# Optimization experiments

Measured on AMD Instinct MI355X. Metric: run time of the kernel, lower is better.

## Reference

```python
import jax, jax.numpy as jnp
import numpy as np

B, S, E, H, V, C = 256, 20, 512, 512, 32000, 1000


def _lstm_step(x, h, c, W, U, b):
    # Keras LSTM, activation='relu', recurrent_activation='sigmoid', gate order i,f,c,o
    z = x @ W + h @ U + b  # (B, 4H)
    i, f, g, o = jnp.split(z, 4, axis=-1)
    i = jax.nn.sigmoid(i)
    f = jax.nn.sigmoid(f)
    g = jax.nn.relu(g)
    o = jax.nn.sigmoid(o)
    c_new = f * c + i * g
    h_new = o * jax.nn.relu(c_new)
    return h_new, c_new


def setup_inputs() -> dict:
    key = jax.random.key(0)
    ks = jax.random.split(key, 24)
    std = 0.05
    d_in1 = S * E + 2 * E  # flattened encoder output + word embed + speaker embed
    inp = {
        "encoded_output": jax.random.normal(ks[0], (B, S, E), jnp.float32),
        "word_embedding": jax.random.normal(ks[1], (B, E), jnp.float32),
        "h0": jax.random.normal(ks[2], (B, H), jnp.float32) * std,
        "c0": jax.random.normal(ks[3], (B, H), jnp.float32) * std,
        "speaker": jax.random.randint(ks[4], (B,), 0, C),
        "addressee": jax.random.randint(ks[5], (B,), 0, C),
        "persona_emb": jax.random.normal(ks[6], (C, E), jnp.float32) * 0.1,
        "W1": jax.random.normal(ks[7], (d_in1, 4 * H), jnp.float32) * std,
        "U1": jax.random.normal(ks[8], (H, 4 * H), jnp.float32) * std,
        "b1": jnp.zeros((4 * H,), jnp.float32),
        "W2": jax.random.normal(ks[9], (H, 4 * H), jnp.float32) * std,
        "U2": jax.random.normal(ks[10], (H, 4 * H), jnp.float32) * std,
        "b2": jnp.zeros((4 * H,), jnp.float32),
        "W3": jax.random.normal(ks[11], (H, 4 * H), jnp.float32) * std,
        "U3": jax.random.normal(ks[12], (H, 4 * H), jnp.float32) * std,
        "b3": jnp.zeros((4 * H,), jnp.float32),
        "W4": jax.random.normal(ks[13], (H, 4 * H), jnp.float32) * std,
        "U4": jax.random.normal(ks[14], (H, 4 * H), jnp.float32) * std,
        "b4": jnp.zeros((4 * H,), jnp.float32),
        "Wd": jax.random.normal(ks[15], (H, V), jnp.float32) * std,
        "bd": jnp.zeros((V,), jnp.float32),
    }
    return inp


def reference(encoded_output, word_embedding, h0, c0, speaker, addressee,
              persona_emb, W1, U1, b1, W2, U2, b2, W3, U3, b3, W4, U4, b4, Wd, bd):
    b = encoded_output.shape[0]
    # The Python double loop in the original is exactly: (B,S,E) -> (B, S*E)
    enc_flat = encoded_output.reshape(b, -1)
    speaker_embed = persona_emb[speaker]  # (B, E)
    # is_speaker=True branch: concat [flattened encoder, word embed, speaker embed]
    x = jnp.concatenate([enc_flat, word_embedding, speaker_embed], axis=-1)
    # seq length is 1, so each LSTM layer is a single cell step;
    # each layer's initial state is the previous layer's final (h, c)
    h1, c1 = _lstm_step(x, h0, c0, W1, U1, b1)
    h2, c2 = _lstm_step(h1, h1, c1, W2, U2, b2)
    h3, c3 = _lstm_step(h2, h2, c2, W3, U3, b3)
    h4, c4 = _lstm_step(h3, h3, c3, W4, U4, b4)
    probs = jax.nn.softmax(h4 @ Wd + bd, axis=-1)  # (B, V)
    return probs, (h4, c4)
```

## Files before the change

### kernel.cpp

```cpp
#include <hip/hip_runtime.h>
#include <cstdint>
#include <cmath>

typedef _Float16 f16;
typedef _Float16 f16x8 __attribute__((ext_vector_type(8)));
typedef _Float16 f16x4 __attribute__((ext_vector_type(4)));
typedef float f32x4 __attribute__((ext_vector_type(4)));

__device__ inline void gld_lds16(const void* g, void* l) {
  __builtin_amdgcn_global_load_lds(
      (__attribute__((address_space(1))) void*)(uintptr_t)g,
      (__attribute__((address_space(3))) void*)l, 16, 0, 0);
}

__global__ __launch_bounds__(256) void build_x1_kernel(
    const float* __restrict__ enc, const float* __restrict__ word,
    const float* __restrict__ pers, const int* __restrict__ speaker,
    const float* __restrict__ h0, f16* __restrict__ X)
{
  const int b  = blockIdx.y;
  const int k2 = blockIdx.x * 256 + threadIdx.x;
  const int k  = k2 * 2;
  float v0, v1;
  if (k < 10240) {
    const float* p = enc + (long long)b * 10240 + k; v0 = p[0]; v1 = p[1];
  } else if (k < 10752) {
    const float* p = word + b * 512 + (k - 10240);   v0 = p[0]; v1 = p[1];
  } else if (k < 11264) {
    const float* p = pers + (long long)speaker[b] * 512 + (k - 10752); v0 = p[0]; v1 = p[1];
  } else {
    const float* p = h0 + b * 512 + (k - 11264);     v0 = p[0]; v1 = p[1];
  }
  union { f16 h[2]; unsigned int u; } pk;
  pk.h[0] = (f16)v0; pk.h[1] = (f16)v1;
  ((unsigned int*)X)[(long long)b * 5888 + k2] = pk.u;
}

__global__ __launch_bounds__(256) void wsum_t_kernel(
    const float* __restrict__ W2, const float* __restrict__ U2,
    const float* __restrict__ W3, const float* __restrict__ U3,
    const float* __restrict__ W4, const float* __restrict__ U4,
    f16* __restrict__ out)
{
  const int t = blockIdx.x * 256 + threadIdx.x;
  const int L = blockIdx.y;
  const float* W = (L == 0) ? W2 : (L == 1) ? W3 : W4;
  const float* U = (L == 0) ? U2 : (L == 1) ? U3 : U4;
  const int n  = t & 2047;
  const int k0 = (t >> 11) << 6;
  f16* op = out + (long long)L * (2048 * 512) + (long long)n * 512 + k0;
  for (int kk = 0; kk < 64; kk += 8) {
    f16x8 v;
    #pragma unroll
    for (int j = 0; j < 8; j++) {
      const int k = k0 + kk + j;
      v[j] = (f16)(W[(long long)k * 2048 + n] + U[(long long)k * 2048 + n]);
    }
    *(f16x8*)(op + kk) = v;
  }
}

__global__ __launch_bounds__(256, 2) void gemm_pipe2(
    const f16* __restrict__ A, int lda,
    const float* __restrict__ B0, const float* __restrict__ B1, int ksw, int ldb,
    void* __restrict__ Cv, int ldc, long long c_split_stride, int niter,
    int store_f16)
{
  __shared__ __align__(16) f16 Ah[2][256 * 32];
  __shared__ __align__(16) f16 Bh[2][128 * 40];

  const int tid  = threadIdx.x;
  const int lane = tid & 63;
  const int wave = tid >> 6;
  const int n0 = blockIdx.x * 128;
  const int kbeg = blockIdx.y * (niter * 32);

  const int a_row16 = lane >> 2;
  const int a_ksub  = ((lane & 3) ^ ((lane >> 3) & 3)) * 8;

  const int nl0  = (tid & 63) * 2;
  const int koct = tid >> 6;

  float2 bv[8];

  auto issueB = [&](int kt) {
    const int kb = kbeg + kt * 32 + koct * 8;
    #pragma unroll
    for (int i = 0; i < 8; i++) {
      const int krow = kb + i;
      const float* bp = (krow >= ksw) ? (B1 + (long long)(krow - ksw) * ldb)
                                      : (B0 + (long long)krow * ldb);
      bv[i] = *(const float2*)(bp + n0 + nl0);
    }
  };
  auto issueA = [&](int kt) {
    const int akb = kbeg + kt * 32;
    #pragma unroll
    for (int half = 0; half < 4; half++) {
      const int rb = wave * 64 + half * 16;
      const f16* gp = A + (long long)(rb + a_row16) * lda + akb + a_ksub;
      gld_lds16((const void*)gp, (void*)&Ah[kt & 1][rb * 32]);
    }
  };
  auto writeB = [&](int kt) {
    f16x8 p0, p1;
    #pragma unroll
    for (int i = 0; i < 8; i++) { p0[i] = (f16)bv[i].x; p1[i] = (f16)bv[i].y; }
    *(f16x8*)&Bh[kt & 1][(nl0    ) * 40 + koct * 8] = p0;
    *(f16x8*)&Bh[kt & 1][(nl0 + 1) * 40 + koct * 8] = p1;
  };

  const int wm = (wave & 1) * 128;
  const int wn = (wave >> 1) * 64;
  f32x4 acc[8][4] = {};

  issueB(0); issueA(0); writeB(0);
  __syncthreads();

  for (int kt = 0; kt < niter; kt++) {
    const int buf = kt & 1;
    const bool more = (kt + 1 < niter);
    if (more) { issueB(kt + 1); issueA(kt + 1); }

    f16x8 bf[4];
    #pragma unroll
    for (int ni = 0; ni < 4; ni++) {
      const int n = wn + ni * 16 + (lane & 15);
      bf[ni] = *(const f16x8*)&Bh[buf][n * 40 + (lane >> 4) * 8];
    }
    #pragma unroll
    for (int mi = 0; mi < 8; mi++) {
      const int m = wm + mi * 16 + (lane & 15);
      const f16x8 af = *(const f16x8*)&Ah[buf][m * 32 + (((lane >> 4) ^ ((m >> 1) & 3)) * 8)];
      #pragma unroll
      for (int ni = 0; ni < 4; ni++)
        acc[mi][ni] = __builtin_amdgcn_mfma_f32_16x16x32_f16(af, bf[ni], acc[mi][ni], 0, 0, 0);
    }

    if (more) writeB(kt + 1);
    __syncthreads();
  }

  if (store_f16) {
    f16* Cs = (f16*)Cv + (long long)blockIdx.y * c_split_stride;
    #pragma unroll
    for (int mi = 0; mi < 8; mi++) {
      const int r0 = wm + mi * 16 + (lane >> 4) * 4;
      #pragma unroll
      for (int ni = 0; ni < 4; ni++) {
        const int cc = n0 + wn + ni * 16 + (lane & 15);
        #pragma unroll
        for (int r = 0; r < 4; r++)
          Cs[(long long)(r0 + r) * ldc + cc] = (f16)acc[mi][ni][r];
      }
    }
  } else {
    float* Cs = (float*)Cv + (long long)blockIdx.y * c_split_stride;
    #pragma unroll
    for (int mi = 0; mi < 8; mi++) {
      const int r0 = wm + mi * 16 + (lane >> 4) * 4;
      #pragma unroll
      for (int ni = 0; ni < 4; ni++) {
        const int cc = n0 + wn + ni * 16 + (lane & 15);
        #pragma unroll
        for (int r = 0; r < 4; r++)
          Cs[(long long)(r0 + r) * ldc + cc] = acc[mi][ni][r];
      }
    }
  }
}

__global__ __launch_bounds__(64) void lstm_small_layer(
    const f16* __restrict__ h_in,
    const f16* __restrict__ WsT,
    const float* __restrict__ bias,
    const float* __restrict__ c_prev, float* __restrict__ c_out,
    f16* __restrict__ h16_out, float* __restrict__ h32_out)
{
  const int lane = threadIdx.x;
  const int wid  = blockIdx.x;
  const int jt = wid & 31, mt = wid >> 5;
  const int m0 = mt * 16, j0 = jt * 16;
  const int lj = lane & 15, quad = lane >> 4;

  const f16* Ab = h_in + (long long)(m0 + lj) * 512 + quad * 8;
  const f16* Bb = WsT + (long long)(j0 + lj) * 512 + quad * 8;
  const long long GS = 512LL * 512;

  f32x4 g0 = {}, g1 = {}, g2 = {}, g3 = {};

  f16x8 ca = *(const f16x8*)(Ab);
  f16x8 cb0 = *(const f16x8*)(Bb);
  f16x8 cb1 = *(const f16x8*)(Bb + GS);
  f16x8 cb2 = *(const f16x8*)(Bb + 2 * GS);
  f16x8 cb3 = *(const f16x8*)(Bb + 3 * GS);

  #pragma unroll
  for (int kt = 0; kt < 16; kt++) {
    f16x8 na = ca, nb0 = cb0, nb1 = cb1, nb2 = cb2, nb3 = cb3;
    if (kt < 15) {
      const int k = (kt + 1) * 32;
      na  = *(const f16x8*)(Ab + k);
      nb0 = *(const f16x8*)(Bb + k);
      nb1 = *(const f16x8*)(Bb + GS + k);
      nb2 = *(const f16x8*)(Bb + 2 * GS + k);
      nb3 = *(const f16x8*)(Bb + 3 * GS + k);
    }
    g0 = __builtin_amdgcn_mfma_f32_16x16x32_f16(ca, cb0, g0, 0, 0, 0);
    g1 = __builtin_amdgcn_mfma_f32_16x16x32_f16(ca, cb1, g1, 0, 0, 0);
    g2 = __builtin_amdgcn_mfma_f32_16x16x32_f16(ca, cb2, g2, 0, 0, 0);
    g3 = __builtin_amdgcn_mfma_f32_16x16x32_f16(ca, cb3, g3, 0, 0, 0);
    ca = na; cb0 = nb0; cb1 = nb1; cb2 = nb2; cb3 = nb3;
  }

  const float bi = bias[j0 + lj],        bfv = bias[512 + j0 + lj];
  const float bg = bias[1024 + j0 + lj], bo  = bias[1536 + j0 + lj];
  #pragma unroll
  for (int r = 0; r < 4; r++) {
    const int m = m0 + quad * 4 + r;
    const int idx = m * 512 + j0 + lj;
    const float gi = 1.f / (1.f + expf(-(g0[r] + bi)));
    const float gf = 1.f / (1.f + expf(-(g1[r] + bfv)));
    const float gg = fmaxf(g2[r] + bg, 0.f);
    const float go = 1.f / (1.f + expf(-(g3[r] + bo)));
    const float cn = gf * c_prev[idx] + gi * gg;
    const float hn = go * fmaxf(cn, 0.f);
    c_out[idx] = cn;
    h16_out[idx] = (f16)hn;
    if (h32_out) h32_out[idx] = hn;
  }
}

__global__ __launch_bounds__(256) void gate_kernel(
    const unsigned int* __restrict__ zbase, int nsplit,
    const float* __restrict__ bias,
    const float* __restrict__ c_prev, float* __restrict__ c_out,
    f16* __restrict__ h16_out)
{
  const int idx2 = blockIdx.x * 256 + threadIdx.x;
  const int b  = idx2 >> 8;
  const int j2 = idx2 & 255;
  const int j  = j2 * 2;
  float z[4][2];
  #pragma unroll
  for (int g = 0; g < 4; g++) { z[g][0] = bias[g * 512 + j]; z[g][1] = bias[g * 512 + j + 1]; }
  #pragma unroll 2
  for (int s = 0; s < nsplit; s++) {
    const unsigned int* zp = zbase + (long long)s * 262144 + b * 1024;
    #pragma unroll
    for (int g = 0; g < 4; g++) {
      union { unsigned int u; f16 h[2]; } v;
      v.u = zp[g * 256 + j2];
      z[g][0] += (float)v.h[0];
      z[g][1] += (float)v.h[1];
    }
  }
  #pragma unroll
  for (int e = 0; e < 2; e++) {
    const float gi = 1.f / (1.f + expf(-z[0][e]));
    const float gf = 1.f / (1.f + expf(-z[1][e]));
    const float gg = fmaxf(z[2][e], 0.f);
    const float go = 1.f / (1.f + expf(-z[3][e]));
    const int idx = b * 512 + j + e;
    const float cn = gf * c_prev[idx] + gi * gg;
    const float hn = go * fmaxf(cn, 0.f);
    c_out[idx] = cn;
    h16_out[idx] = (f16)hn;
  }
}

__global__ __launch_bounds__(1024) void softmax_kernel(
    const f16* __restrict__ zdec, float* __restrict__ out,
    const float* __restrict__ bd)
{
  const int row = blockIdx.x;
  const int t = threadIdx.x;
  const f16x4* p0 = (const f16x4*)(zdec + (long long)row * 32000);
  const f16x4* p1 = (const f16x4*)(zdec + 8192000LL + (long long)row * 32000);
  float4* rp = (float4*)(out + (long long)row * 32000);
  const float4* bp = (const float4*)bd;
  float4 l[8];
  float m = -1e30f;
  #pragma unroll
  for (int i = 0; i < 8; i++) {
    const int v = t + i * 1024;
    if (v < 8000) {
      const f16x4 a = p0[v], b = p1[v];
      const float4 bb = bp[v];
      float4 x;
      x.x = (float)a[0] + (float)b[0] + bb.x;
      x.y = (float)a[1] + (float)b[1] + bb.y;
      x.z = (float)a[2] + (float)b[2] + bb.z;
      x.w = (float)a[3] + (float)b[3] + bb.w;
      l[i] = x;
      m = fmaxf(m, fmaxf(fmaxf(x.x, x.y), fmaxf(x.z, x.w)));
    } else {
      l[i] = make_float4(-1e30f, -1e30f, -1e30f, -1e30f);
    }
  }
  #pragma unroll
  for (int off = 32; off > 0; off >>= 1) m = fmaxf(m, __shfl_xor(m, off, 64));
  __shared__ float redm[16];
  __shared__ float reds[16];
  const int w = t >> 6;
  if ((t & 63) == 0) redm[w] = m;
  __syncthreads();
  float bm = redm[0];
  #pragma unroll
  for (int i = 1; i < 16; i++) bm = fmaxf(bm, redm[i]);
  float s = 0.f;
  #pragma unroll
  for (int i = 0; i < 8; i++) {
    const float ex = expf(l[i].x - bm), ey = expf(l[i].y - bm);
    const float ez = expf(l[i].z - bm), ew = expf(l[i].w - bm);
    l[i] = make_float4(ex, ey, ez, ew);
    s += (ex + ey) + (ez + ew);
  }
  #pragma unroll
  for (int off = 32; off > 0; off >>= 1) s += __shfl_xor(s, off, 64);
  if ((t & 63) == 0) reds[w] = s;
  __syncthreads();
  float ts = 0.f;
  #pragma unroll
  for (int i = 0; i < 16; i++) ts += reds[i];
  const float inv = 1.0f / ts;
  #pragma unroll
  for (int i = 0; i < 8; i++) {
    const int v = t + i * 1024;
    if (v < 8000) {
      float4 x = l[i];
      x.x *= inv; x.y *= inv; x.z *= inv; x.w *= inv;
      rp[v] = x;
    }
  }
}

extern "C" void kernel_launch(void* const* d_in, const int* in_sizes, int n_in,
                              void* d_out, int out_size, void* d_ws, size_t ws_size,
                              hipStream_t stream) {
  const float* enc     = (const float*)d_in[0];
  const float* word    = (const float*)d_in[1];
  const float* h0      = (const float*)d_in[2];
  const float* c0      = (const float*)d_in[3];
  const int*   speaker = (const int*)d_in[4];
  const float* pers = (const float*)d_in[6];
  const float* W1 = (const float*)d_in[7];
  const float* U1 = (const float*)d_in[8];
  const float* b1 = (const float*)d_in[9];
  const float* W2 = (const float*)d_in[10];
  const float* U2 = (const float*)d_in[11];
  const float* b2 = (const float*)d_in[12];
  const float* W3 = (const float*)d_in[13];
  const float* U3 = (const float*)d_in[14];
  const float* b3 = (const float*)d_in[15];
  const float* W4 = (const float*)d_in[16];
  const float* U4 = (const float*)d_in[17];
  const float* b4 = (const float*)d_in[18];
  const float* Wd = (const float*)d_in[19];
  const float* bd = (const float*)d_in[20];

  float* out = (float*)d_out;
  float* h4_out = out + 8192000;
  float* c4_out = out + 8192000 + 131072;

  f16*   hA   = (f16*)d_ws;
  f16*   hB   = (f16*)((char*)d_ws + 262144);
  f16*   hC   = (f16*)((char*)d_ws + 524288);
  float* cbuf = (float*)((char*)d_ws + 786432);
  f16*   WsT  = (f16*)((char*)d_ws + 2097152);
  f16*   X1h  = (f16*)((char*)d_ws + 8388608);
  f16*   zp16 = (f16*)((char*)d_ws + 16777216);
  f16*   zdec = (f16*)((char*)d_ws + 100663296);

  const int BIG = 1 << 29;
  const long long LW = 2048LL * 512;

  build_x1_kernel<<<dim3(23, 256), 256, 0, stream>>>(enc, word, pers, speaker, h0, X1h);
  wsum_t_kernel<<<dim3(64, 3), 256, 0, stream>>>(W2, U2, W3, U3, W4, U4, WsT);

  gemm_pipe2<<<dim3(16, 46), 256, 0, stream>>>(
      X1h, 11776, W1, U1, 11264, 2048, zp16, 2048, 524288LL, 8, 1);
  gate_kernel<<<dim3(256), 256, 0, stream>>>((const unsigned int*)zp16, 46, b1, c0, cbuf, hA);

  lstm_small_layer<<<dim3(512), 64, 0, stream>>>(hA, WsT,          b2, cbuf, cbuf, hB, nullptr);
  lstm_small_layer<<<dim3(512), 64, 0, stream>>>(hB, WsT + LW,     b3, cbuf, cbuf, hA, nullptr);
  lstm_small_layer<<<dim3(512), 64, 0, stream>>>(hA, WsT + 2 * LW, b4, cbuf, c4_out, hC, h4_out);

  gemm_pipe2<<<dim3(250, 2), 256, 0, stream>>>(
      hC, 512, Wd, Wd, BIG, 32000, zdec, 32000, 8192000LL, 8, 1);

  softmax_kernel<<<dim3(256), 1024, 0, stream>>>(zdec, out, bd);
}
```

Measured before the change: 342.9 us.

## Remap GEMM blocks per XCD and halve split-K partitions

The GEMM kernel now takes a flat 1D grid and maps block IDs to output tiles and K-splits so that blocks on the same XCD (blockIdx & 7) share K slices or contiguous N tiles, which should improve L2 locality of the streamed fp32 weights. The first-layer GEMM goes from 46 to 23 K-splits with twice the iterations each, and the decoder GEMM drops its 2-way split-K, so the softmax reads one partial instead of two. This cuts partial-sum traffic and reduction work. The cost is fewer blocks in flight for the decoder GEMM (250 tiles), some idle blocks in the padded grid, and longer per-block K loops.

```diff
diff --git a/kernel.cpp b/kernel.cpp
--- a/kernel.cpp
+++ b/kernel.cpp
@@ -64,16 +64,33 @@
     const f16* __restrict__ A, int lda,
     const float* __restrict__ B0, const float* __restrict__ B1, int ksw, int ldb,
     void* __restrict__ Cv, int ldc, long long c_split_stride, int niter,
-    int store_f16)
+    int store_f16, int NT, int NS)
 {
   __shared__ __align__(16) f16 Ah[2][256 * 32];
   __shared__ __align__(16) f16 Bh[2][128 * 40];
+
+  const int f   = blockIdx.x;
+  const int xcd = f & 7;
+  const int j   = f >> 3;
+  int nt, s;
+  if (NS > 1) {
+    const int g = j / NT;
+    nt = j - g * NT;
+    s  = g * 8 + xcd;
+    if (s >= NS) return;
+  } else {
+    const int chunk = (NT + 7) >> 3;
+    if (j >= chunk) return;
+    nt = xcd * chunk + j;
+    if (nt >= NT) return;
+    s = 0;
+  }
 
   const int tid  = threadIdx.x;
   const int lane = tid & 63;
   const int wave = tid >> 6;
-  const int n0 = blockIdx.x * 128;
-  const int kbeg = blockIdx.y * (niter * 32);
+  const int n0 = nt * 128;
+  const int kbeg = s * (niter * 32);
 
   const int a_row16 = lane >> 2;
   const int a_ksub  = ((lane & 3) ^ ((lane >> 3) & 3)) * 8;
@@ -142,7 +159,7 @@
   }
 
   if (store_f16) {
-    f16* Cs = (f16*)Cv + (long long)blockIdx.y * c_split_stride;
+    f16* Cs = (f16*)Cv + (long long)s * c_split_stride;
     #pragma unroll
     for (int mi = 0; mi < 8; mi++) {
       const int r0 = wm + mi * 16 + (lane >> 4) * 4;
@@ -155,7 +172,7 @@
       }
     }
   } else {
-    float* Cs = (float*)Cv + (long long)blockIdx.y * c_split_stride;
+    float* Cs = (float*)Cv + (long long)s * c_split_stride;
     #pragma unroll
     for (int mi = 0; mi < 8; mi++) {
       const int r0 = wm + mi * 16 + (lane >> 4) * 4;
@@ -276,7 +293,6 @@
   const int row = blockIdx.x;
   const int t = threadIdx.x;
   const f16x4* p0 = (const f16x4*)(zdec + (long long)row * 32000);
-  const f16x4* p1 = (const f16x4*)(zdec + 8192000LL + (long long)row * 32000);
   float4* rp = (float4*)(out + (long long)row * 32000);
   const float4* bp = (const float4*)bd;
   float4 l[8];
@@ -285,13 +301,13 @@
   for (int i = 0; i < 8; i++) {
     const int v = t + i * 1024;
     if (v < 8000) {
-      const f16x4 a = p0[v], b = p1[v];
+      const f16x4 a = p0[v];
       const float4 bb = bp[v];
       float4 x;
-      x.x = (float)a[0] + (float)b[0] + bb.x;
-      x.y = (float)a[1] + (float)b[1] + bb.y;
-      x.z = (float)a[2] + (float)b[2] + bb.z;
-      x.w = (float)a[3] + (float)b[3] + bb.w;
+      x.x = (float)a[0] + bb.x;
+      x.y = (float)a[1] + bb.y;
+      x.z = (float)a[2] + bb.z;
+      x.w = (float)a[3] + bb.w;
       l[i] = x;
       m = fmaxf(m, fmaxf(fmaxf(x.x, x.y), fmaxf(x.z, x.w)));
     } else {
@@ -370,7 +386,7 @@
   f16*   WsT  = (f16*)((char*)d_ws + 2097152);
   f16*   X1h  = (f16*)((char*)d_ws + 8388608);
   f16*   zp16 = (f16*)((char*)d_ws + 16777216);
-  f16*   zdec = (f16*)((char*)d_ws + 100663296);
+  f16*   zdec = (f16*)((char*)d_ws + 50331648);
 
   const int BIG = 1 << 29;
   const long long LW = 2048LL * 512;
@@ -378,16 +394,16 @@
   build_x1_kernel<<<dim3(23, 256), 256, 0, stream>>>(enc, word, pers, speaker, h0, X1h);
   wsum_t_kernel<<<dim3(64, 3), 256, 0, stream>>>(W2, U2, W3, U3, W4, U4, WsT);
 
-  gemm_pipe2<<<dim3(16, 46), 256, 0, stream>>>(
-      X1h, 11776, W1, U1, 11264, 2048, zp16, 2048, 524288LL, 8, 1);
-  gate_kernel<<<dim3(256), 256, 0, stream>>>((const unsigned int*)zp16, 46, b1, c0, cbuf, hA);
+  gemm_pipe2<<<dim3(384), 256, 0, stream>>>(
+      X1h, 11776, W1, U1, 11264, 2048, zp16, 2048, 524288LL, 16, 1, 16, 23);
+  gate_kernel<<<dim3(256), 256, 0, stream>>>((const unsigned int*)zp16, 23, b1, c0, cbuf, hA);
 
   lstm_small_layer<<<dim3(512), 64, 0, stream>>>(hA, WsT,          b2, cbuf, cbuf, hB, nullptr);
   lstm_small_layer<<<dim3(512), 64, 0, stream>>>(hB, WsT + LW,     b3, cbuf, cbuf, hA, nullptr);
   lstm_small_layer<<<dim3(512), 64, 0, stream>>>(hA, WsT + 2 * LW, b4, cbuf, c4_out, hC, h4_out);
 
-  gemm_pipe2<<<dim3(250, 2), 256, 0, stream>>>(
-      hC, 512, Wd, Wd, BIG, 32000, zdec, 32000, 8192000LL, 8, 1);
+  gemm_pipe2<<<dim3(256), 256, 0, stream>>>(
+      hC, 512, Wd, Wd, BIG, 32000, zdec, 32000, 0LL, 16, 1, 250, 1);
 
   softmax_kernel<<<dim3(256), 1024, 0, stream>>>(zdec, out, bd);
 }
```

Measured after the change: 331.5 us. 3.3% less time.
